# Performance work log

Hardware: AMD Instinct MI355X
Metric: run time of the kernel (lower is better)

## Reference

```python
import jax, jax.numpy as jnp
import numpy as np

# Per-type input feature dims (NODE_DIM values); max dim = 128 = padded width of x.
NODE_DIMS = np.array([16, 32, 64, 128, 64, 32, 16, 128], dtype=np.int32)
N_TYPES = 8
MAX_DIM = 128
FEAT = 256          # node_feature_dim
N_GRAPHS = 100000   # batch_size; one node of each type per graph


def setup_inputs() -> dict:
    key = jax.random.key(0)
    k1, k2, k3 = jax.random.split(key, 3)
    num_nodes = N_GRAPHS * N_TYPES
    x = jax.random.normal(k1, (num_nodes, MAX_DIM), dtype=jnp.float32)
    # Per-type Linear weights, padded to MAX_DIM on the input axis.
    W = jax.random.normal(k2, (N_TYPES, FEAT, MAX_DIM), dtype=jnp.float32) * 0.05
    b = jax.random.normal(k3, (N_TYPES, FEAT), dtype=jnp.float32) * 0.05
    return {"x": x, "W": W, "b": b}


def reference(x, W, b):
    # Node n = g*N_TYPES + k is the type-k node of graph g (the gather index
    # ptr[b] + node_name.index(k) in the original). Dropout is eval-mode (identity).
    # Mask weight columns beyond each type's true input dim: equivalent to
    # slicing x[:, :NODE_DIM[k]] before the per-type Linear.
    mask = (jnp.arange(MAX_DIM)[None, None, :] < jnp.asarray(NODE_DIMS)[:, None, None]).astype(x.dtype)  # [T,1,D]
    W_eff = W * mask  # [T,F,D]
    xg = x.reshape(N_GRAPHS, N_TYPES, MAX_DIM)  # [G,T,D]
    y = jnp.einsum("gtd,tfd->gtf", xg, W_eff) + b[None, :, :]  # [G,T,F]
    return y.reshape(N_GRAPHS * N_TYPES, FEAT)
```

## Files before the change

kernel.cpp:

```cpp
#include <hip/hip_runtime.h>
#include <hip/hip_bf16.h>

#define N_GRAPHS 100000
#define NT 8
#define MAXD 128
#define FEAT 256

typedef __attribute__((ext_vector_type(8))) short short8;
typedef __attribute__((ext_vector_type(4))) float f32x4;

__device__ __forceinline__ unsigned short f2bf(float f) {
    unsigned u = __builtin_bit_cast(unsigned, f);
    u = (u + 0x7fffu + ((u >> 16) & 1u)) >> 16;
    return (unsigned short)u;
}

template<int KS>
__global__ __launch_bounds__(256)
void node_enc_kernel(const float* __restrict__ x,
                     const float* __restrict__ W,
                     const float* __restrict__ bias_g,
                     float* __restrict__ out,
                     int tmap, int dmap)
{
    constexpr int K32 = KS * 32;
    const int t   = (tmap >> (8 * blockIdx.y)) & 0xff;
    const int dim = (dmap >> (8 * blockIdx.y)) & 0xff;
    const int tid  = threadIdx.x;
    const int lane = tid & 63;
    const int wave = tid >> 6;
    const int n0   = wave * 64;
    const int cgrp = lane >> 4;
    const int c16  = lane & 15;

    __shared__ unsigned short As[64][136];

    short8 Bf[KS][4];
    float bias[4];
    const float* Wt = W + (size_t)t * FEAT * MAXD;
    #pragma unroll
    for (int nt = 0; nt < 4; ++nt) {
        const int col = n0 + nt * 16 + c16;
        bias[nt] = bias_g[t * FEAT + col];
        #pragma unroll
        for (int ks = 0; ks < KS; ++ks) {
            const int k = ks * 32 + cgrp * 8;
            const float* wp = Wt + (size_t)col * MAXD + k;
            f32x4 w0 = *(const f32x4*)wp;
            f32x4 w1 = *(const f32x4*)(wp + 4);
            short8 s;
            #pragma unroll
            for (int j = 0; j < 4; ++j) {
                s[j]     = (k + j     < dim) ? (short)f2bf(w0[j]) : (short)0;
                s[j + 4] = (k + j + 4 < dim) ? (short)f2bf(w1[j]) : (short)0;
            }
            Bf[ks][nt] = s;
        }
    }

    const int grow0 = blockIdx.x * 64;

    {
        constexpr int TPR = K32 / 8;
        constexpr int RPP = 256 / TPR;
        constexpr int PASSES = 64 / RPP;
        const int rloc = tid / TPR;
        const int kg   = tid % TPR;
        #pragma unroll
        for (int p = 0; p < PASSES; ++p) {
            const int i = p * RPP + rloc;
            const int g = grow0 + i;
            f32x4 v0 = {0.f,0.f,0.f,0.f}, v1 = {0.f,0.f,0.f,0.f};
            if (g < N_GRAPHS) {
                const float* rp = x + ((size_t)g * NT + t) * MAXD + kg * 8;
                v0 = *(const f32x4*)rp;
                v1 = *(const f32x4*)(rp + 4);
            }
            short8 s;
            #pragma unroll
            for (int j = 0; j < 4; ++j) {
                s[j]     = (short)f2bf(v0[j]);
                s[j + 4] = (short)f2bf(v1[j]);
            }
            *(short8*)&As[i][kg * 8] = s;
        }
    }
    __syncthreads();

    #pragma unroll
    for (int ms = 0; ms < 4; ++ms) {
        short8 a[KS];
        #pragma unroll
        for (int ks = 0; ks < KS; ++ks)
            a[ks] = *(const short8*)&As[ms * 16 + c16][ks * 32 + cgrp * 8];

        f32x4 acc[4] = {{0,0,0,0},{0,0,0,0},{0,0,0,0},{0,0,0,0}};
        #pragma unroll
        for (int ks = 0; ks < KS; ++ks) {
            #pragma unroll
            for (int nt = 0; nt < 4; ++nt)
                acc[nt] = __builtin_amdgcn_mfma_f32_16x16x32_bf16(a[ks], Bf[ks][nt], acc[nt], 0, 0, 0);
        }

        #pragma unroll
        for (int nt = 0; nt < 4; ++nt) {
            const int col = n0 + nt * 16 + c16;
            #pragma unroll
            for (int r = 0; r < 4; ++r) {
                const int g = grow0 + ms * 16 + cgrp * 4 + r;
                if (g < N_GRAPHS)
                    out[((size_t)g * NT + t) * FEAT + col] = acc[nt][r] + bias[nt];
            }
        }
    }
}

extern "C" void kernel_launch(void* const* d_in, const int* in_sizes, int n_in,
                              void* d_out, int out_size, void* d_ws, size_t ws_size,
                              hipStream_t stream)
{
    const float* x = (const float*)d_in[0];
    const float* W = (const float*)d_in[1];
    const float* b = (const float*)d_in[2];
    float* out = (float*)d_out;

    const int chunks = (N_GRAPHS + 63) / 64;

    node_enc_kernel<1><<<dim3(chunks, 4), 256, 0, stream>>>(x, W, b, out,
        0 | (1 << 8) | (5 << 16) | (6 << 24),
        16 | (32 << 8) | (32 << 16) | (16 << 24));
    node_enc_kernel<2><<<dim3(chunks, 2), 256, 0, stream>>>(x, W, b, out,
        2 | (4 << 8), 64 | (64 << 8));
    node_enc_kernel<4><<<dim3(chunks, 2), 256, 0, stream>>>(x, W, b, out,
        3 | (7 << 8), 128 | (128 << 8));
}
```

Baseline: 346.8 us.

## Double rows per block, skip padded x loads, use nontemporal loads/stores

Each block now handles 128 graph rows instead of 64, so the per-type weight fragments are loaded and converted half as often. The shared tile is sized to the actual K width. Loads of x columns beyond the type's true dim are skipped and zero-filled. Global loads and output stores use nontemporal hints, and a bounds-check-free store path is used for full tiles. Launch bounds request 4 blocks per CU; larger tiles mean fewer blocks and possibly less latency hiding.

```diff
diff --git a/kernel.cpp b/kernel.cpp
--- a/kernel.cpp
+++ b/kernel.cpp
@@ -16,14 +16,15 @@
 }
 
 template<int KS>
-__global__ __launch_bounds__(256)
+__global__ __launch_bounds__(256, 4)
 void node_enc_kernel(const float* __restrict__ x,
                      const float* __restrict__ W,
                      const float* __restrict__ bias_g,
                      float* __restrict__ out,
                      int tmap, int dmap)
 {
-    constexpr int K32 = KS * 32;
+    constexpr int K32  = KS * 32;
+    constexpr int ROWS = 128;
     const int t   = (tmap >> (8 * blockIdx.y)) & 0xff;
     const int dim = (dmap >> (8 * blockIdx.y)) & 0xff;
     const int tid  = threadIdx.x;
@@ -33,7 +34,7 @@
     const int cgrp = lane >> 4;
     const int c16  = lane & 15;
 
-    __shared__ unsigned short As[64][136];
+    __shared__ unsigned short As[ROWS][K32 + 8];
 
     short8 Bf[KS][4];
     float bias[4];
@@ -58,23 +59,24 @@
         }
     }
 
-    const int grow0 = blockIdx.x * 64;
+    const int grow0 = blockIdx.x * ROWS;
 
     {
-        constexpr int TPR = K32 / 8;
-        constexpr int RPP = 256 / TPR;
-        constexpr int PASSES = 64 / RPP;
+        constexpr int TPR    = K32 / 8;
+        constexpr int RPP    = 256 / TPR;
+        constexpr int PASSES = ROWS / RPP;
         const int rloc = tid / TPR;
         const int kg   = tid % TPR;
+        const bool kload = (kg * 8 < dim);
         #pragma unroll
         for (int p = 0; p < PASSES; ++p) {
             const int i = p * RPP + rloc;
             const int g = grow0 + i;
             f32x4 v0 = {0.f,0.f,0.f,0.f}, v1 = {0.f,0.f,0.f,0.f};
-            if (g < N_GRAPHS) {
+            if (kload && g < N_GRAPHS) {
                 const float* rp = x + ((size_t)g * NT + t) * MAXD + kg * 8;
-                v0 = *(const f32x4*)rp;
-                v1 = *(const f32x4*)(rp + 4);
+                v0 = __builtin_nontemporal_load((const f32x4*)rp);
+                v1 = __builtin_nontemporal_load((const f32x4*)rp + 1);
             }
             short8 s;
             #pragma unroll
@@ -87,8 +89,10 @@
     }
     __syncthreads();
 
+    const bool full = (grow0 + ROWS <= N_GRAPHS);
+
     #pragma unroll
-    for (int ms = 0; ms < 4; ++ms) {
+    for (int ms = 0; ms < ROWS / 16; ++ms) {
         short8 a[KS];
         #pragma unroll
         for (int ks = 0; ks < KS; ++ks)
@@ -102,14 +106,28 @@
                 acc[nt] = __builtin_amdgcn_mfma_f32_16x16x32_bf16(a[ks], Bf[ks][nt], acc[nt], 0, 0, 0);
         }
 
-        #pragma unroll
-        for (int nt = 0; nt < 4; ++nt) {
-            const int col = n0 + nt * 16 + c16;
+        if (full) {
             #pragma unroll
-            for (int r = 0; r < 4; ++r) {
-                const int g = grow0 + ms * 16 + cgrp * 4 + r;
-                if (g < N_GRAPHS)
-                    out[((size_t)g * NT + t) * FEAT + col] = acc[nt][r] + bias[nt];
+            for (int nt = 0; nt < 4; ++nt) {
+                const int col = n0 + nt * 16 + c16;
+                #pragma unroll
+                for (int r = 0; r < 4; ++r) {
+                    const int g = grow0 + ms * 16 + cgrp * 4 + r;
+                    __builtin_nontemporal_store(acc[nt][r] + bias[nt],
+                        &out[((size_t)g * NT + t) * FEAT + col]);
+                }
+            }
+        } else {
+            #pragma unroll
+            for (int nt = 0; nt < 4; ++nt) {
+                const int col = n0 + nt * 16 + c16;
+                #pragma unroll
+                for (int r = 0; r < 4; ++r) {
+                    const int g = grow0 + ms * 16 + cgrp * 4 + r;
+                    if (g < N_GRAPHS)
+                        __builtin_nontemporal_store(acc[nt][r] + bias[nt],
+                            &out[((size_t)g * NT + t) * FEAT + col]);
+                }
             }
         }
     }
@@ -124,7 +142,7 @@
     const float* b = (const float*)d_in[2];
     float* out = (float*)d_out;
 
-    const int chunks = (N_GRAPHS + 63) / 64;
+    const int chunks = (N_GRAPHS + 127) / 128;
 
     node_enc_kernel<1><<<dim3(chunks, 4), 256, 0, stream>>>(x, W, b, out,
         0 | (1 << 8) | (5 << 16) | (6 << 24),
```

Result: faster. 339.8 us (-2.0%).
